# Kernel tuning notes

Measured on AMD Instinct MI355X. Metric: run time of the kernel, lower is better.

## Reference

```python
import jax, jax.numpy as jnp
import numpy as np

NUM_HEADS = 16
HEAD_DIM = 64
CONTEXT = 128


def setup_inputs() -> dict:
    key = jax.random.key(0)
    k1, k2, k3, k4, k5 = jax.random.split(key, 5)
    B, S, H = 4, 4096, 1024
    inputs = jax.random.normal(k1, (B, S, H), dtype=jnp.float32)
    attention_mask = jnp.ones((B, S), dtype=jnp.int32)
    s = 1.0 / np.sqrt(H)
    Wq = jax.random.normal(k2, (H, H), dtype=jnp.float32) * s
    Wk = jax.random.normal(k3, (H, H), dtype=jnp.float32) * s
    Wv = jax.random.normal(k4, (H, H), dtype=jnp.float32) * s
    Wo = jax.random.normal(k5, (H, H), dtype=jnp.float32) * s
    return {"inputs": inputs, "attention_mask": attention_mask,
            "Wq": Wq, "Wk": Wk, "Wv": Wv, "Wo": Wo}


def reference(inputs, attention_mask, Wq, Wk, Wv, Wo):
    B, S, H = inputs.shape
    nH, dh = NUM_HEADS, HEAD_DIM
    C = min(CONTEXT, S)
    ctx_start = max(0, S - C)
    scale = 1.0 / np.sqrt(dh)

    # Q from all positions; K/V only from the recent context window
    q = (inputs @ Wq.T).reshape(B, S, nH, dh).transpose(0, 2, 1, 3)      # [B,nH,S,dh]
    ctx_in = inputs[:, ctx_start:, :]                                    # [B,C,H]
    k = (ctx_in @ Wk.T).reshape(B, C, nH, dh).transpose(0, 2, 1, 3)      # [B,nH,C,dh]
    v = (ctx_in @ Wv.T).reshape(B, C, nH, dh).transpose(0, 2, 1, 3)      # [B,nH,C,dh]

    scores = jnp.einsum('bhsd,bhcd->bhsc', q, k) * scale                 # [B,nH,S,C]

    # causal mask: context position <= query position; queries strictly
    # before the context window may attend to the first context token
    qpos = jnp.arange(S)
    cpos = jnp.arange(ctx_start, ctx_start + C)
    causal = cpos[None, :] <= qpos[:, None]                              # [S,C]
    before = qpos < ctx_start
    causal = causal.at[:, 0].set(causal[:, 0] | before)
    mask = causal[None, None, :, :]                                      # [1,1,S,C]

    # padding mask on context tokens
    ctx_pad = (attention_mask[:, ctx_start:ctx_start + C] != 0)          # [B,C]
    mask = mask & ctx_pad[:, None, None, :]

    scores = jnp.where(mask, scores, -jnp.inf)
    weights = jax.nn.softmax(scores, axis=-1)

    out = jnp.einsum('bhsc,bhcd->bhsd', weights, v)                      # [B,nH,S,dh]
    out = out.transpose(0, 2, 1, 3).reshape(B, S, H)
    return out @ Wo.T
```

## Files before the change

### kernel.cpp

```cpp
#include <hip/hip_runtime.h>
#include <math.h>

#define B_ 4
#define S_ 4096
#define H_ 1024
#define NH 16
#define DH 64
#define CTX 128
#define CSTART (S_ - CTX)
#define KDIM 1024
#define KH 512

typedef __attribute__((ext_vector_type(8))) short short8;
typedef __attribute__((ext_vector_type(4))) float floatx4;
typedef unsigned short ushort_t;

__device__ inline unsigned short f2bf(float x) {
    union { float f; unsigned u; } v; v.f = x;
    unsigned r = v.u + 0x7fffu + ((v.u >> 16) & 1u);
    return (unsigned short)(r >> 16);
}

__device__ inline uint4 pack8(float4 a, float4 b) {
    union { unsigned short us[8]; uint4 u4; } p;
    p.us[0]=f2bf(a.x); p.us[1]=f2bf(a.y); p.us[2]=f2bf(a.z); p.us[3]=f2bf(a.w);
    p.us[4]=f2bf(b.x); p.us[5]=f2bf(b.y); p.us[6]=f2bf(b.z); p.us[7]=f2bf(b.w);
    return p.u4;
}

__device__ inline float4 add4(float4 a, float4 b) {
    float4 r; r.x=a.x+b.x; r.y=a.y+b.y; r.z=a.z+b.z; r.w=a.w+b.w; return r;
}

#define GLOAD_LDS16(g, l) \
    __builtin_amdgcn_global_load_lds((__attribute__((address_space(1))) const void*)(g), \
                                     (__attribute__((address_space(3))) void*)(l), 16, 0, 0)

__global__ __launch_bounds__(256) void prep(const float* __restrict__ in,
                                            const float* __restrict__ Wq, const float* __restrict__ Wk,
                                            const float* __restrict__ Wv, const float* __restrict__ Wo,
                                            ushort_t* __restrict__ Wbf, ushort_t* __restrict__ Xs) {
    int bx = blockIdx.x;
    if (bx < 2048) {
        size_t idx = (size_t)bx * 256 + threadIdx.x;
        size_t e = idx * 8;
        int wsel = (int)(e >> 20);
        size_t off = e & 1048575;
        const float* src = wsel == 0 ? Wq : wsel == 1 ? Wk : wsel == 2 ? Wv : Wo;
        const float4* s4 = (const float4*)(src + off);
        *(uint4*)(Wbf + e) = pack8(s4[0], s4[1]);
    } else {
        int idx = (bx - 2048) * 256 + threadIdx.x;
        int e = idx * 8;
        int m = e >> 10;
        int col = e & 1023;
        int b = m >> 7, i = m & 127;
        const float4* s4 = (const float4*)(in + (size_t)(b * S_ + CSTART + i) * H_ + col);
        *(uint4*)(Xs + e) = pack8(s4[0], s4[1]);
    }
}

__global__ __launch_bounds__(256) void gemm_part(const ushort_t* __restrict__ A,
                                                 const ushort_t* __restrict__ W,
                                                 float* __restrict__ P, int N) {
    __shared__ ushort_t As[64][64];
    __shared__ ushort_t Bs[64][64];
    int tid = threadIdx.x;
    int lane = tid & 63, w = tid >> 6;
    int m0 = blockIdx.y * 64, n0 = blockIdx.x * 64;
    int ks = blockIdx.z;
    int f0 = tid, f1 = tid + 256;
    int r0 = f0 >> 3, g0 = (f0 & 7) ^ (r0 & 7);
    int r1 = f1 >> 3, g1 = (f1 & 7) ^ (r1 & 7);
    const ushort_t* ga0 = A + (size_t)(m0 + r0) * KDIM + ks * KH + g0 * 8;
    const ushort_t* ga1 = A + (size_t)(m0 + r1) * KDIM + ks * KH + g1 * 8;
    const ushort_t* gb0 = W + (size_t)(n0 + r0) * KDIM + ks * KH + g0 * 8;
    const ushort_t* gb1 = W + (size_t)(n0 + r1) * KDIM + ks * KH + g1 * 8;
    char* la0 = (char*)As + f0 * 16;
    char* la1 = (char*)As + f1 * 16;
    char* lb0 = (char*)Bs + f0 * 16;
    char* lb1 = (char*)Bs + f1 * 16;
    int fm = lane & 15, q = lane >> 4;
    int wr = w >> 1, wc = w & 1;
    int ma0 = wr * 32, na0 = wc * 32;
    floatx4 acc[2][2] = {};
    for (int k0 = 0; k0 < KH; k0 += 64) {
        GLOAD_LDS16(ga0 + k0, la0);
        GLOAD_LDS16(ga1 + k0, la1);
        GLOAD_LDS16(gb0 + k0, lb0);
        GLOAD_LDS16(gb1 + k0, lb1);
        __syncthreads();
        #pragma unroll
        for (int kb = 0; kb < 2; kb++) {
            short8 af[2], bfr[2];
            #pragma unroll
            for (int t = 0; t < 2; t++) {
                int m = ma0 + t * 16 + fm;
                int pa = (kb * 4 + q) ^ (m & 7);
                af[t] = *(const short8*)&As[m][pa * 8];
                int n = na0 + t * 16 + fm;
                int pb = (kb * 4 + q) ^ (n & 7);
                bfr[t] = *(const short8*)&Bs[n][pb * 8];
            }
            #pragma unroll
            for (int i = 0; i < 2; i++)
                #pragma unroll
                for (int j = 0; j < 2; j++)
                    acc[i][j] = __builtin_amdgcn_mfma_f32_16x16x32_bf16(af[i], bfr[j], acc[i][j], 0, 0, 0);
        }
        __syncthreads();
    }
    float* outp = P + (size_t)ks * 512 * N;
    #pragma unroll
    for (int i = 0; i < 2; i++)
        #pragma unroll
        for (int j = 0; j < 2; j++) {
            int row = m0 + ma0 + i * 16 + q * 4;
            int col = n0 + na0 + j * 16 + fm;
            #pragma unroll
            for (int t = 0; t < 4; t++)
                outp[(size_t)(row + t) * N + col] = acc[i][j][t];
        }
}

__global__ __launch_bounds__(256) void attn(const float* __restrict__ Pq,
                                            const int* __restrict__ amask,
                                            ushort_t* __restrict__ AO) {
    __shared__ __align__(16) char smem[46080];
    ushort_t* Qs   = (ushort_t*)(smem);
    ushort_t* Ksh  = (ushort_t*)(smem + 9216);
    ushort_t* Pb   = (ushort_t*)(smem);
    float*    linv = (float*)(smem + 27648);
    int*      amk  = (int*)(smem + 27904);
    ushort_t* Vt   = (ushort_t*)(smem + 28416);

    int gid = blockIdx.x;
    int b = gid >> 5, h = (gid >> 1) & 15, half = gid & 1;
    int tid = threadIdx.x;
    int cmax = half ? CTX : 64;
    {
        int r = tid >> 2, ch = tid & 3;
        size_t qb = (size_t)(b * CTX + half * 64 + r) * 3072 + h * 64 + ch * 16;
        const float4* q0 = (const float4*)(Pq + qb);
        const float4* q1 = (const float4*)(Pq + (size_t)512 * 3072 + qb);
        float4 a0 = add4(q0[0], q1[0]), a1 = add4(q0[1], q1[1]);
        float4 a2 = add4(q0[2], q1[2]), a3 = add4(q0[3], q1[3]);
        *(uint4*)(Qs + r * 72 + ch * 16)     = pack8(a0, a1);
        *(uint4*)(Qs + r * 72 + ch * 16 + 8) = pack8(a2, a3);
        for (int idx = tid; idx < cmax * 4; idx += 256) {
            int kr = idx >> 2, kch = idx & 3;
            size_t base = (size_t)(b * CTX + kr) * 3072 + h * 64 + kch * 16;
            const float4* p0 = (const float4*)(Pq + base);
            const float4* p1 = (const float4*)(Pq + (size_t)512 * 3072 + base);
            float4 k0 = add4(p0[256], p1[256]), k1 = add4(p0[257], p1[257]);
            float4 k2 = add4(p0[258], p1[258]), k3 = add4(p0[259], p1[259]);
            *(uint4*)(Ksh + kr * 72 + kch * 16)     = pack8(k0, k1);
            *(uint4*)(Ksh + kr * 72 + kch * 16 + 8) = pack8(k2, k3);
            float vv[16];
            #pragma unroll
            for (int c4 = 0; c4 < 4; c4++) {
                float4 s = add4(p0[512 + c4], p1[512 + c4]);
                vv[c4*4+0]=s.x; vv[c4*4+1]=s.y; vv[c4*4+2]=s.z; vv[c4*4+3]=s.w;
            }
            #pragma unroll
            for (int i = 0; i < 16; i++)
                Vt[(kch * 16 + i) * 136 + kr] = f2bf(vv[i]);
        }
        if (tid < 128) amk[tid] = amask[b * S_ + CSTART + tid];
    }
    __syncthreads();

    int w = tid >> 6, lane = tid & 63;
    int qt = half * 4 + w;
    int lr0 = w * 16;
    int fm = lane & 15, quad = lane >> 4;

    short8 af[2];
    #pragma unroll
    for (int kb = 0; kb < 2; kb++)
        af[kb] = *(const short8*)(Qs + (lr0 + fm) * 72 + kb * 32 + quad * 8);
    floatx4 acc[8] = {};
    for (int ct = 0; ct <= qt; ct++) {
        #pragma unroll
        for (int kb = 0; kb < 2; kb++) {
            short8 bfr = *(const short8*)(Ksh + (ct * 16 + fm) * 72 + kb * 32 + quad * 8);
            acc[ct] = __builtin_amdgcn_mfma_f32_16x16x32_bf16(af[kb], bfr, acc[ct], 0, 0, 0);
        }
    }
    int myamk[8];
    #pragma unroll
    for (int ct = 0; ct < 8; ct++) myamk[ct] = amk[ct * 16 + fm];
    float ls[4];
    #pragma unroll
    for (int t = 0; t < 4; t++) {
        int row = qt * 16 + quad * 4 + t;
        float m = -INFINITY;
        #pragma unroll
        for (int ct = 0; ct < 8; ct++) {
            int col = ct * 16 + fm;
            float s = acc[ct][t] * 0.125f;
            bool valid = (ct <= qt) && (col <= row) && (myamk[ct] != 0);
            if (valid) m = fmaxf(m, s);
        }
        #pragma unroll
        for (int off = 8; off >= 1; off >>= 1) m = fmaxf(m, __shfl_xor(m, off, 64));
        float l = 0.f;
        #pragma unroll
        for (int ct = 0; ct < 8; ct++) {
            int col = ct * 16 + fm;
            float s = acc[ct][t] * 0.125f;
            bool valid = (ct <= qt) && (col <= row) && (myamk[ct] != 0);
            float p = valid ? __expf(s - m) : 0.f;
            acc[ct][t] = p;
            l += p;
        }
        #pragma unroll
        for (int off = 8; off >= 1; off >>= 1) l += __shfl_xor(l, off, 64);
        ls[t] = l;
    }
    __syncthreads();
    #pragma unroll
    for (int t = 0; t < 4; t++) {
        int lrow = lr0 + quad * 4 + t;
        #pragma unroll
        for (int ct = 0; ct < 8; ct++)
            Pb[lrow * 136 + ct * 16 + fm] = f2bf(acc[ct][t]);
        if (fm == 0) linv[lrow] = 1.f / ls[t];
    }
    int kmax = (qt >> 1) + 1;
    floatx4 oacc[4] = {};
    for (int kb = 0; kb < kmax; kb++) {
        short8 paf = *(const short8*)(Pb + (lr0 + fm) * 136 + kb * 32 + quad * 8);
        #pragma unroll
        for (int dt = 0; dt < 4; dt++) {
            short8 vbf = *(const short8*)(Vt + (dt * 16 + fm) * 136 + kb * 32 + quad * 8);
            oacc[dt] = __builtin_amdgcn_mfma_f32_16x16x32_bf16(paf, vbf, oacc[dt], 0, 0, 0);
        }
    }
    #pragma unroll
    for (int t = 0; t < 4; t++) {
        int lrow = lr0 + quad * 4 + t;
        int grow = qt * 16 + quad * 4 + t;
        float inv = linv[lrow];
        #pragma unroll
        for (int dt = 0; dt < 4; dt++)
            AO[(size_t)(b * CTX + grow) * H_ + h * 64 + dt * 16 + fm] = f2bf(oacc[dt][t] * inv);
    }
}

__global__ __launch_bounds__(256) void assemble(const float* __restrict__ Po,
                                                float* __restrict__ out) {
    size_t idx = (size_t)blockIdx.x * 256 + threadIdx.x;
    int row = (int)(idx >> 8);
    int c4  = (int)(idx & 255);
    int b = row >> 12;
    int p = row & 4095;
    int lr = (p < CSTART) ? 0 : (p - CSTART);
    size_t o = (size_t)(b * CTX + lr) * H_ + c4 * 4;
    float4 v0 = *(const float4*)(Po + o);
    float4 v1 = *(const float4*)(Po + (size_t)512 * H_ + o);
    ((float4*)out)[idx] = add4(v0, v1);
}

extern "C" void kernel_launch(void* const* d_in, const int* in_sizes, int n_in,
                              void* d_out, int out_size, void* d_ws, size_t ws_size,
                              hipStream_t stream) {
    const float* inputs = (const float*)d_in[0];
    const int*   amask  = (const int*)d_in[1];
    const float* Wq     = (const float*)d_in[2];
    const float* Wk     = (const float*)d_in[3];
    const float* Wv     = (const float*)d_in[4];
    const float* Wo     = (const float*)d_in[5];
    float* out = (float*)d_out;

    char* ws = (char*)d_ws;
    ushort_t* Xs   = (ushort_t*)(ws);
    ushort_t* Wbf  = (ushort_t*)(ws + (1u << 20));
    float*    Pq   = (float*)(ws + (9u << 20));
    ushort_t* AObf = (ushort_t*)(ws + (23u << 20));
    float*    Po   = (float*)(ws + (24u << 20));

    prep<<<2304, 256, 0, stream>>>(inputs, Wq, Wk, Wv, Wo, Wbf, Xs);

    dim3 gq(3072 / 64, 512 / 64, 2);
    gemm_part<<<gq, 256, 0, stream>>>(Xs, Wbf, Pq, 3072);

    attn<<<128, 256, 0, stream>>>(Pq, amask, AObf);

    dim3 go(1024 / 64, 512 / 64, 2);
    gemm_part<<<go, 256, 0, stream>>>(AObf, Wbf + (size_t)3072 * 1024, Po, 1024);

    assemble<<<16384, 256, 0, stream>>>(Po, out);
}
```

Before: 151.8 us.

## Fuse all stages into one cooperative persistent kernel with grid syncs

Replaces the five separate launches (prep, QKV GEMM, attention, output GEMM, assemble) with a single cooperative kernel of 512 blocks that separates the phases with grid.sync(). The output projection now runs the full K=1024 in one tile and writes straight into the context rows of the output, so the split-K partial buffer and its reduction disappear. The final phase broadcasts the position-0 context row to every earlier position. This removes launch gaps and one intermediate buffer, but adds grid-wide barrier costs, leaves most blocks idle during the attention and output phases, and needs all 512 blocks to be co-resident.

```diff
diff --git a/kernel.cpp b/kernel.cpp
--- a/kernel.cpp
+++ b/kernel.cpp
@@ -1,5 +1,8 @@
 #include <hip/hip_runtime.h>
+#include <hip/hip_cooperative_groups.h>
 #include <math.h>
+
+namespace cg = cooperative_groups;
 
 #define B_ 4
 #define S_ 4096
@@ -36,55 +39,32 @@
     __builtin_amdgcn_global_load_lds((__attribute__((address_space(1))) const void*)(g), \
                                      (__attribute__((address_space(3))) void*)(l), 16, 0, 0)
 
-__global__ __launch_bounds__(256) void prep(const float* __restrict__ in,
-                                            const float* __restrict__ Wq, const float* __restrict__ Wk,
-                                            const float* __restrict__ Wv, const float* __restrict__ Wo,
-                                            ushort_t* __restrict__ Wbf, ushort_t* __restrict__ Xs) {
-    int bx = blockIdx.x;
-    if (bx < 2048) {
-        size_t idx = (size_t)bx * 256 + threadIdx.x;
-        size_t e = idx * 8;
-        int wsel = (int)(e >> 20);
-        size_t off = e & 1048575;
-        const float* src = wsel == 0 ? Wq : wsel == 1 ? Wk : wsel == 2 ? Wv : Wo;
-        const float4* s4 = (const float4*)(src + off);
-        *(uint4*)(Wbf + e) = pack8(s4[0], s4[1]);
-    } else {
-        int idx = (bx - 2048) * 256 + threadIdx.x;
-        int e = idx * 8;
-        int m = e >> 10;
-        int col = e & 1023;
-        int b = m >> 7, i = m & 127;
-        const float4* s4 = (const float4*)(in + (size_t)(b * S_ + CSTART + i) * H_ + col);
-        *(uint4*)(Xs + e) = pack8(s4[0], s4[1]);
-    }
-}
-
-__global__ __launch_bounds__(256) void gemm_part(const ushort_t* __restrict__ A,
-                                                 const ushort_t* __restrict__ W,
-                                                 float* __restrict__ P, int N) {
-    __shared__ ushort_t As[64][64];
-    __shared__ ushort_t Bs[64][64];
-    int tid = threadIdx.x;
+template<bool DIRECT, int KLEN>
+__device__ __forceinline__ void gemm_tile(const ushort_t* __restrict__ A,
+                                          const ushort_t* __restrict__ W,
+                                          float* __restrict__ P, int N,
+                                          int m0, int n0, int koff,
+                                          char* smem, int tid) {
+    ushort_t* As = (ushort_t*)smem;
+    ushort_t* Bs = As + 4096;
     int lane = tid & 63, w = tid >> 6;
-    int m0 = blockIdx.y * 64, n0 = blockIdx.x * 64;
-    int ks = blockIdx.z;
     int f0 = tid, f1 = tid + 256;
     int r0 = f0 >> 3, g0 = (f0 & 7) ^ (r0 & 7);
     int r1 = f1 >> 3, g1 = (f1 & 7) ^ (r1 & 7);
-    const ushort_t* ga0 = A + (size_t)(m0 + r0) * KDIM + ks * KH + g0 * 8;
-    const ushort_t* ga1 = A + (size_t)(m0 + r1) * KDIM + ks * KH + g1 * 8;
-    const ushort_t* gb0 = W + (size_t)(n0 + r0) * KDIM + ks * KH + g0 * 8;
-    const ushort_t* gb1 = W + (size_t)(n0 + r1) * KDIM + ks * KH + g1 * 8;
-    char* la0 = (char*)As + f0 * 16;
-    char* la1 = (char*)As + f1 * 16;
-    char* lb0 = (char*)Bs + f0 * 16;
-    char* lb1 = (char*)Bs + f1 * 16;
+    const ushort_t* ga0 = A + (size_t)(m0 + r0) * KDIM + koff + g0 * 8;
+    const ushort_t* ga1 = A + (size_t)(m0 + r1) * KDIM + koff + g1 * 8;
+    const ushort_t* gb0 = W + (size_t)(n0 + r0) * KDIM + koff + g0 * 8;
+    const ushort_t* gb1 = W + (size_t)(n0 + r1) * KDIM + koff + g1 * 8;
+    char* la0 = smem + f0 * 16;
+    char* la1 = smem + f1 * 16;
+    char* lb0 = smem + 8192 + f0 * 16;
+    char* lb1 = smem + 8192 + f1 * 16;
     int fm = lane & 15, q = lane >> 4;
     int wr = w >> 1, wc = w & 1;
     int ma0 = wr * 32, na0 = wc * 32;
     floatx4 acc[2][2] = {};
-    for (int k0 = 0; k0 < KH; k0 += 64) {
+    #pragma unroll
+    for (int k0 = 0; k0 < KLEN; k0 += 64) {
         GLOAD_LDS16(ga0 + k0, la0);
         GLOAD_LDS16(ga1 + k0, la1);
         GLOAD_LDS16(gb0 + k0, lb0);
@@ -97,10 +77,10 @@
             for (int t = 0; t < 2; t++) {
                 int m = ma0 + t * 16 + fm;
                 int pa = (kb * 4 + q) ^ (m & 7);
-                af[t] = *(const short8*)&As[m][pa * 8];
+                af[t] = *(const short8*)(As + m * 64 + pa * 8);
                 int n = na0 + t * 16 + fm;
                 int pb = (kb * 4 + q) ^ (n & 7);
-                bfr[t] = *(const short8*)&Bs[n][pb * 8];
+                bfr[t] = *(const short8*)(Bs + n * 64 + pb * 8);
             }
             #pragma unroll
             for (int i = 0; i < 2; i++)
@@ -110,7 +90,6 @@
         }
         __syncthreads();
     }
-    float* outp = P + (size_t)ks * 512 * N;
     #pragma unroll
     for (int i = 0; i < 2; i++)
         #pragma unroll
@@ -118,15 +97,22 @@
             int row = m0 + ma0 + i * 16 + q * 4;
             int col = n0 + na0 + j * 16 + fm;
             #pragma unroll
-            for (int t = 0; t < 4; t++)
-                outp[(size_t)(row + t) * N + col] = acc[i][j][t];
-        }
-}
-
-__global__ __launch_bounds__(256) void attn(const float* __restrict__ Pq,
-                                            const int* __restrict__ amask,
-                                            ushort_t* __restrict__ AO) {
-    __shared__ __align__(16) char smem[46080];
+            for (int t = 0; t < 4; t++) {
+                int rr = row + t;
+                if (DIRECT) {
+                    size_t gr = (size_t)((rr >> 7) * S_ + CSTART + (rr & 127));
+                    P[gr * 1024 + col] = acc[i][j][t];
+                } else {
+                    P[(size_t)rr * N + col] = acc[i][j][t];
+                }
+            }
+        }
+}
+
+__device__ __forceinline__ void attn_body(const float* __restrict__ Pq,
+                                          const int* __restrict__ amask,
+                                          ushort_t* __restrict__ AO,
+                                          char* smem, int gid) {
     ushort_t* Qs   = (ushort_t*)(smem);
     ushort_t* Ksh  = (ushort_t*)(smem + 9216);
     ushort_t* Pb   = (ushort_t*)(smem);
@@ -134,7 +120,6 @@
     int*      amk  = (int*)(smem + 27904);
     ushort_t* Vt   = (ushort_t*)(smem + 28416);
 
-    int gid = blockIdx.x;
     int b = gid >> 5, h = (gid >> 1) & 15, half = gid & 1;
     int tid = threadIdx.x;
     int cmax = half ? CTX : 64;
@@ -248,18 +233,67 @@
     }
 }
 
-__global__ __launch_bounds__(256) void assemble(const float* __restrict__ Po,
+__global__ __launch_bounds__(256, 2) void fused(const float* __restrict__ in,
+                                                const int* __restrict__ amask,
+                                                const float* __restrict__ Wq, const float* __restrict__ Wk,
+                                                const float* __restrict__ Wv, const float* __restrict__ Wo,
+                                                ushort_t* __restrict__ Wbf, ushort_t* __restrict__ Xs,
+                                                float* __restrict__ Pq, ushort_t* __restrict__ AObf,
                                                 float* __restrict__ out) {
-    size_t idx = (size_t)blockIdx.x * 256 + threadIdx.x;
-    int row = (int)(idx >> 8);
-    int c4  = (int)(idx & 255);
-    int b = row >> 12;
-    int p = row & 4095;
-    int lr = (p < CSTART) ? 0 : (p - CSTART);
-    size_t o = (size_t)(b * CTX + lr) * H_ + c4 * 4;
-    float4 v0 = *(const float4*)(Po + o);
-    float4 v1 = *(const float4*)(Po + (size_t)512 * H_ + o);
-    ((float4*)out)[idx] = add4(v0, v1);
+    __shared__ __align__(16) char smem[46080];
+    cg::grid_group grid = cg::this_grid();
+    int bid = blockIdx.x, tid = threadIdx.x;
+
+    for (unsigned u = (unsigned)bid * 256 + tid; u < 589824u; u += 131072u) {
+        size_t e = (size_t)u * 8;
+        if (u < 524288u) {
+            int wsel = (int)(e >> 20);
+            size_t off = e & 1048575;
+            const float* src = wsel == 0 ? Wq : wsel == 1 ? Wk : wsel == 2 ? Wv : Wo;
+            const float4* s4 = (const float4*)(src + off);
+            *(uint4*)(Wbf + e) = pack8(s4[0], s4[1]);
+        } else {
+            size_t e2 = e - 4194304;
+            int m = (int)(e2 >> 10), col = (int)(e2 & 1023);
+            int b2 = m >> 7, i = m & 127;
+            const float4* s4 = (const float4*)(in + (size_t)(b2 * S_ + CSTART + i) * H_ + col);
+            *(uint4*)(Xs + e2) = pack8(s4[0], s4[1]);
+        }
+    }
+    grid.sync();
+
+    {
+        int job = bid;
+        int x = job % 48, y = (job / 48) & 7, z = job / 384;
+        gemm_tile<false, KH>(Xs, Wbf, Pq + (size_t)z * 512 * 3072, 3072,
+                             y * 64, x * 64, z * KH, smem, tid);
+        if (bid < 256) {
+            int j2 = bid + 512;
+            int x2 = j2 % 48, y2 = (j2 / 48) & 7, z2 = j2 / 384;
+            gemm_tile<false, KH>(Xs, Wbf, Pq + (size_t)z2 * 512 * 3072, 3072,
+                                 y2 * 64, x2 * 64, z2 * KH, smem, tid);
+        }
+    }
+    grid.sync();
+
+    if (bid < 128) attn_body(Pq, amask, AObf, smem, bid);
+    grid.sync();
+
+    if (bid < 128) {
+        int x = bid % 16, y = bid / 16;
+        gemm_tile<true, 1024>(AObf, Wbf + (size_t)3072 * 1024, out, 1024,
+                              y * 64, x * 64, 0, smem, tid);
+    }
+    grid.sync();
+
+    for (unsigned idx = (unsigned)bid * 256 + tid; idx < 4063232u; idx += 131072u) {
+        unsigned b2 = idx / 1015808u;
+        unsigned rem = idx - b2 * 1015808u;
+        unsigned p = rem >> 8;
+        unsigned c4 = rem & 255u;
+        float4 v = *(const float4*)(out + (size_t)(b2 * S_ + CSTART) * H_ + c4 * 4);
+        ((float4*)out)[(size_t)(b2 * S_ + p) * 256 + c4] = v;
+    }
 }
 
 extern "C" void kernel_launch(void* const* d_in, const int* in_sizes, int n_in,
@@ -278,17 +312,19 @@
     ushort_t* Wbf  = (ushort_t*)(ws + (1u << 20));
     float*    Pq   = (float*)(ws + (9u << 20));
     ushort_t* AObf = (ushort_t*)(ws + (23u << 20));
-    float*    Po   = (float*)(ws + (24u << 20));
-
-    prep<<<2304, 256, 0, stream>>>(inputs, Wq, Wk, Wv, Wo, Wbf, Xs);
-
-    dim3 gq(3072 / 64, 512 / 64, 2);
-    gemm_part<<<gq, 256, 0, stream>>>(Xs, Wbf, Pq, 3072);
-
-    attn<<<128, 256, 0, stream>>>(Pq, amask, AObf);
-
-    dim3 go(1024 / 64, 512 / 64, 2);
-    gemm_part<<<go, 256, 0, stream>>>(AObf, Wbf + (size_t)3072 * 1024, Po, 1024);
-
-    assemble<<<16384, 256, 0, stream>>>(Po, out);
-}
+
+    void* args[11];
+    args[0]  = (void*)&inputs;
+    args[1]  = (void*)&amask;
+    args[2]  = (void*)&Wq;
+    args[3]  = (void*)&Wk;
+    args[4]  = (void*)&Wv;
+    args[5]  = (void*)&Wo;
+    args[6]  = (void*)&Wbf;
+    args[7]  = (void*)&Xs;
+    args[8]  = (void*)&Pq;
+    args[9]  = (void*)&AObf;
+    args[10] = (void*)&out;
+
+    hipLaunchCooperativeKernel((const void*)fused, dim3(512), dim3(256), args, 0, stream);
+}
```

After: 406.6 us. 2.68x slower.

## Fuse bf16 conversion into GEMMs and fuse output projection with broadcast write

Applied to the files above, without the earlier changes.

Drops the separate prep kernel and converts fp32 inputs and weights to bf16 while staging tiles into shared memory, using register prefetch of the next k-tile. The output projection now runs over the full K in one pass and writes the 512 context rows straight into the output. Extra blocks compute the single shared row for pre-context positions as a dot-product GEMV and broadcast it across those rows, which removes the split-K partial buffer and the assemble kernel. In exchange the GEMM loops do conversion work inline, and the broadcast rows use a scalar per-element bf16 path.

```diff
diff --git a/kernel.cpp b/kernel.cpp
--- a/kernel.cpp
+++ b/kernel.cpp
@@ -9,7 +9,6 @@
 #define CTX 128
 #define CSTART (S_ - CTX)
 #define KDIM 1024
-#define KH 512
 
 typedef __attribute__((ext_vector_type(8))) short short8;
 typedef __attribute__((ext_vector_type(4))) float floatx4;
@@ -19,6 +18,10 @@
     union { float f; unsigned u; } v; v.f = x;
     unsigned r = v.u + 0x7fffu + ((v.u >> 16) & 1u);
     return (unsigned short)(r >> 16);
+}
+
+__device__ inline float bf2f(ushort_t u) {
+    union { unsigned u; float f; } v; v.u = ((unsigned)u) << 16; return v.f;
 }
 
 __device__ inline uint4 pack8(float4 a, float4 b) {
@@ -36,60 +39,56 @@
     __builtin_amdgcn_global_load_lds((__attribute__((address_space(1))) const void*)(g), \
                                      (__attribute__((address_space(3))) void*)(l), 16, 0, 0)
 
-__global__ __launch_bounds__(256) void prep(const float* __restrict__ in,
-                                            const float* __restrict__ Wq, const float* __restrict__ Wk,
-                                            const float* __restrict__ Wv, const float* __restrict__ Wo,
-                                            ushort_t* __restrict__ Wbf, ushort_t* __restrict__ Xs) {
-    int bx = blockIdx.x;
-    if (bx < 2048) {
-        size_t idx = (size_t)bx * 256 + threadIdx.x;
-        size_t e = idx * 8;
-        int wsel = (int)(e >> 20);
-        size_t off = e & 1048575;
-        const float* src = wsel == 0 ? Wq : wsel == 1 ? Wk : wsel == 2 ? Wv : Wo;
-        const float4* s4 = (const float4*)(src + off);
-        *(uint4*)(Wbf + e) = pack8(s4[0], s4[1]);
-    } else {
-        int idx = (bx - 2048) * 256 + threadIdx.x;
-        int e = idx * 8;
-        int m = e >> 10;
-        int col = e & 1023;
-        int b = m >> 7, i = m & 127;
-        const float4* s4 = (const float4*)(in + (size_t)(b * S_ + CSTART + i) * H_ + col);
-        *(uint4*)(Xs + e) = pack8(s4[0], s4[1]);
-    }
-}
-
-__global__ __launch_bounds__(256) void gemm_part(const ushort_t* __restrict__ A,
-                                                 const ushort_t* __restrict__ W,
-                                                 float* __restrict__ P, int N) {
+__global__ __launch_bounds__(256) void qkv_gemm(const float* __restrict__ in,
+                                                const float* __restrict__ Wq,
+                                                const float* __restrict__ Wk,
+                                                const float* __restrict__ Wv,
+                                                float* __restrict__ Pq) {
     __shared__ ushort_t As[64][64];
     __shared__ ushort_t Bs[64][64];
+    int bid = blockIdx.x;
+    int z = bid / 384;
+    int rem = bid - z * 384;
+    int x = rem % 48, y = rem / 48;
+    int m0 = y * 64, n0 = x * 64, koff = z * 512;
+    const float* Wsrc = (n0 < 1024) ? Wq : (n0 < 2048) ? Wk : Wv;
+    int nrow0 = n0 & 1023;
+
     int tid = threadIdx.x;
     int lane = tid & 63, w = tid >> 6;
-    int m0 = blockIdx.y * 64, n0 = blockIdx.x * 64;
-    int ks = blockIdx.z;
-    int f0 = tid, f1 = tid + 256;
-    int r0 = f0 >> 3, g0 = (f0 & 7) ^ (r0 & 7);
-    int r1 = f1 >> 3, g1 = (f1 & 7) ^ (r1 & 7);
-    const ushort_t* ga0 = A + (size_t)(m0 + r0) * KDIM + ks * KH + g0 * 8;
-    const ushort_t* ga1 = A + (size_t)(m0 + r1) * KDIM + ks * KH + g1 * 8;
-    const ushort_t* gb0 = W + (size_t)(n0 + r0) * KDIM + ks * KH + g0 * 8;
-    const ushort_t* gb1 = W + (size_t)(n0 + r1) * KDIM + ks * KH + g1 * 8;
-    char* la0 = (char*)As + f0 * 16;
-    char* la1 = (char*)As + f1 * 16;
-    char* lb0 = (char*)Bs + f0 * 16;
-    char* lb1 = (char*)Bs + f1 * 16;
+    int r0 = tid >> 3, g0 = (tid & 7) ^ (r0 & 7);
+    int r1 = r0 + 32,  g1 = (tid & 7) ^ (r1 & 7);
+
+    int am0 = m0 + r0, am1 = m0 + r1;
+    const float* gaA0 = in + (size_t)((am0 >> 7) * S_ + CSTART + (am0 & 127)) * H_ + koff + g0 * 8;
+    const float* gaA1 = in + (size_t)((am1 >> 7) * S_ + CSTART + (am1 & 127)) * H_ + koff + g1 * 8;
+    const float* gaB0 = Wsrc + (size_t)(nrow0 + r0) * 1024 + koff + g0 * 8;
+    const float* gaB1 = Wsrc + (size_t)(nrow0 + r1) * 1024 + koff + g1 * 8;
+    uint4* lsA0 = (uint4*)((char*)As + tid * 16);
+    uint4* lsA1 = (uint4*)((char*)As + tid * 16 + 4096);
+    uint4* lsB0 = (uint4*)((char*)Bs + tid * 16);
+    uint4* lsB1 = (uint4*)((char*)Bs + tid * 16 + 4096);
+
     int fm = lane & 15, q = lane >> 4;
     int wr = w >> 1, wc = w & 1;
     int ma0 = wr * 32, na0 = wc * 32;
     floatx4 acc[2][2] = {};
-    for (int k0 = 0; k0 < KH; k0 += 64) {
-        GLOAD_LDS16(ga0 + k0, la0);
-        GLOAD_LDS16(ga1 + k0, la1);
-        GLOAD_LDS16(gb0 + k0, lb0);
-        GLOAD_LDS16(gb1 + k0, lb1);
+
+    float4 ra0, ra1, ra2, ra3, rb0, rb1, rb2, rb3;
+#define LOAD_REGS_K1(k) do { \
+        ra0 = *(const float4*)(gaA0 + (k));     ra1 = *(const float4*)(gaA0 + (k) + 4); \
+        ra2 = *(const float4*)(gaA1 + (k));     ra3 = *(const float4*)(gaA1 + (k) + 4); \
+        rb0 = *(const float4*)(gaB0 + (k));     rb1 = *(const float4*)(gaB0 + (k) + 4); \
+        rb2 = *(const float4*)(gaB1 + (k));     rb3 = *(const float4*)(gaB1 + (k) + 4); } while (0)
+
+    LOAD_REGS_K1(0);
+    for (int k0 = 0; k0 < 512; k0 += 64) {
+        uint4 pa0 = pack8(ra0, ra1), pa1 = pack8(ra2, ra3);
+        uint4 pb0 = pack8(rb0, rb1), pb1 = pack8(rb2, rb3);
+        if (k0) __syncthreads();
+        *lsA0 = pa0; *lsA1 = pa1; *lsB0 = pb0; *lsB1 = pb1;
         __syncthreads();
+        if (k0 + 64 < 512) LOAD_REGS_K1(k0 + 64);
         #pragma unroll
         for (int kb = 0; kb < 2; kb++) {
             short8 af[2], bfr[2];
@@ -97,10 +96,10 @@
             for (int t = 0; t < 2; t++) {
                 int m = ma0 + t * 16 + fm;
                 int pa = (kb * 4 + q) ^ (m & 7);
-                af[t] = *(const short8*)&As[m][pa * 8];
+                af[t] = *(const short8*)(&As[m][pa * 8]);
                 int n = na0 + t * 16 + fm;
                 int pb = (kb * 4 + q) ^ (n & 7);
-                bfr[t] = *(const short8*)&Bs[n][pb * 8];
+                bfr[t] = *(const short8*)(&Bs[n][pb * 8]);
             }
             #pragma unroll
             for (int i = 0; i < 2; i++)
@@ -108,9 +107,8 @@
                 for (int j = 0; j < 2; j++)
                     acc[i][j] = __builtin_amdgcn_mfma_f32_16x16x32_bf16(af[i], bfr[j], acc[i][j], 0, 0, 0);
         }
-        __syncthreads();
-    }
-    float* outp = P + (size_t)ks * 512 * N;
+    }
+    float* outp = Pq + (size_t)z * 512 * 3072;
     #pragma unroll
     for (int i = 0; i < 2; i++)
         #pragma unroll
@@ -119,7 +117,7 @@
             int col = n0 + na0 + j * 16 + fm;
             #pragma unroll
             for (int t = 0; t < 4; t++)
-                outp[(size_t)(row + t) * N + col] = acc[i][j][t];
+                outp[(size_t)(row + t) * 3072 + col] = acc[i][j][t];
         }
 }
 
@@ -248,18 +246,120 @@
     }
 }
 
-__global__ __launch_bounds__(256) void assemble(const float* __restrict__ Po,
-                                                float* __restrict__ out) {
-    size_t idx = (size_t)blockIdx.x * 256 + threadIdx.x;
-    int row = (int)(idx >> 8);
-    int c4  = (int)(idx & 255);
-    int b = row >> 12;
-    int p = row & 4095;
-    int lr = (p < CSTART) ? 0 : (p - CSTART);
-    size_t o = (size_t)(b * CTX + lr) * H_ + c4 * 4;
-    float4 v0 = *(const float4*)(Po + o);
-    float4 v1 = *(const float4*)(Po + (size_t)512 * H_ + o);
-    ((float4*)out)[idx] = add4(v0, v1);
+__global__ __launch_bounds__(256) void ogemm_bcast(const ushort_t* __restrict__ AObf,
+                                                   const float* __restrict__ Wo,
+                                                   float* __restrict__ out) {
+    __shared__ __align__(16) char smem[16384];
+    int bid = blockIdx.x;
+    int tid = threadIdx.x;
+
+    if (bid < 128) {
+        ushort_t (*As)[64] = (ushort_t(*)[64])smem;
+        ushort_t (*Bs)[64] = (ushort_t(*)[64])(smem + 8192);
+        int x = bid % 16, y = bid / 16;
+        int m0 = y * 64, n0 = x * 64;
+        int lane = tid & 63, w = tid >> 6;
+        int r0 = tid >> 3, g0 = (tid & 7) ^ (r0 & 7);
+        int r1 = r0 + 32,  g1 = (tid & 7) ^ (r1 & 7);
+        const ushort_t* ga0 = AObf + (size_t)(m0 + r0) * KDIM + g0 * 8;
+        const ushort_t* ga1 = AObf + (size_t)(m0 + r1) * KDIM + g1 * 8;
+        const float*    gb0 = Wo + (size_t)(n0 + r0) * 1024 + g0 * 8;
+        const float*    gb1 = Wo + (size_t)(n0 + r1) * 1024 + g1 * 8;
+        char* laA0 = smem + tid * 16;
+        char* laA1 = smem + tid * 16 + 4096;
+        uint4* lsB0 = (uint4*)(smem + 8192 + tid * 16);
+        uint4* lsB1 = (uint4*)(smem + 8192 + tid * 16 + 4096);
+
+        int fm = lane & 15, q = lane >> 4;
+        int wr = w >> 1, wc = w & 1;
+        int ma0 = wr * 32, na0 = wc * 32;
+        floatx4 acc[2][2] = {};
+
+        float4 rb0, rb1, rb2, rb3;
+#define LOAD_REGS_K3(k) do { \
+            rb0 = *(const float4*)(gb0 + (k)); rb1 = *(const float4*)(gb0 + (k) + 4); \
+            rb2 = *(const float4*)(gb1 + (k)); rb3 = *(const float4*)(gb1 + (k) + 4); } while (0)
+
+        LOAD_REGS_K3(0);
+        for (int k0 = 0; k0 < 1024; k0 += 64) {
+            uint4 pb0 = pack8(rb0, rb1), pb1 = pack8(rb2, rb3);
+            if (k0) __syncthreads();
+            GLOAD_LDS16(ga0 + k0, laA0);
+            GLOAD_LDS16(ga1 + k0, laA1);
+            *lsB0 = pb0; *lsB1 = pb1;
+            __syncthreads();
+            if (k0 + 64 < 1024) LOAD_REGS_K3(k0 + 64);
+            #pragma unroll
+            for (int kb = 0; kb < 2; kb++) {
+                short8 af[2], bfr[2];
+                #pragma unroll
+                for (int t = 0; t < 2; t++) {
+                    int m = ma0 + t * 16 + fm;
+                    int pa = (kb * 4 + q) ^ (m & 7);
+                    af[t] = *(const short8*)(&As[m][pa * 8]);
+                    int n = na0 + t * 16 + fm;
+                    int pb = (kb * 4 + q) ^ (n & 7);
+                    bfr[t] = *(const short8*)(&Bs[n][pb * 8]);
+                }
+                #pragma unroll
+                for (int i = 0; i < 2; i++)
+                    #pragma unroll
+                    for (int j = 0; j < 2; j++)
+                        acc[i][j] = __builtin_amdgcn_mfma_f32_16x16x32_bf16(af[i], bfr[j], acc[i][j], 0, 0, 0);
+            }
+        }
+        #pragma unroll
+        for (int i = 0; i < 2; i++)
+            #pragma unroll
+            for (int j = 0; j < 2; j++) {
+                int row = m0 + ma0 + i * 16 + q * 4;
+                int col = n0 + na0 + j * 16 + fm;
+                #pragma unroll
+                for (int t = 0; t < 4; t++) {
+                    int rr = row + t;
+                    size_t gr = (size_t)((rr >> 7) * S_ + CSTART + (rr & 127));
+                    out[gr * 1024 + col] = acc[i][j][t];
+                }
+            }
+    } else {
+        float* vals = (float*)smem;
+        int idx = bid - 128;
+        int c  = idx & 15;
+        int b2 = (idx >> 4) & 3;
+        int rc = idx >> 6;
+        int n0 = c * 64;
+        int w = tid >> 6, lane = tid & 63;
+        int rsub = lane >> 4, kl = lane & 15;
+        const ushort_t* ao = AObf + (size_t)(b2 * 128) * 1024;
+        #pragma unroll
+        for (int p = 0; p < 4; p++) {
+            int rl = p * 16 + w * 4 + rsub;
+            const float* wrow = Wo + (size_t)(n0 + rl) * 1024;
+            float4 av = {0.f, 0.f, 0.f, 0.f};
+            #pragma unroll
+            for (int it = 0; it < 16; it++) {
+                int k = kl * 4 + it * 64;
+                float4 wv = *(const float4*)(wrow + k);
+                av.x += wv.x * bf2f(ao[k]);
+                av.y += wv.y * bf2f(ao[k + 1]);
+                av.z += wv.z * bf2f(ao[k + 2]);
+                av.w += wv.w * bf2f(ao[k + 3]);
+            }
+            float s = av.x + av.y + av.z + av.w;
+            #pragma unroll
+            for (int off = 1; off < 16; off <<= 1) s += __shfl_xor(s, off, 64);
+            if (kl == 0) vals[rl] = s;
+        }
+        __syncthreads();
+        int c4 = tid & 15, ro = tid >> 4;
+        float4 v4 = *(const float4*)(vals + c4 * 4);
+        size_t gbase = (size_t)b2 * S_ * 1024 + n0 + c4 * 4;
+        #pragma unroll
+        for (int i = 0; i < 31; i++) {
+            int p = rc * 496 + ro + i * 16;
+            *(float4*)(out + gbase + (size_t)p * 1024) = v4;
+        }
+    }
 }
 
 extern "C" void kernel_launch(void* const* d_in, const int* in_sizes, int n_in,
@@ -274,21 +374,10 @@
     float* out = (float*)d_out;
 
     char* ws = (char*)d_ws;
-    ushort_t* Xs   = (ushort_t*)(ws);
-    ushort_t* Wbf  = (ushort_t*)(ws + (1u << 20));
-    float*    Pq   = (float*)(ws + (9u << 20));
-    ushort_t* AObf = (ushort_t*)(ws + (23u << 20));
-    float*    Po   = (float*)(ws + (24u << 20));
-
-    prep<<<2304, 256, 0, stream>>>(inputs, Wq, Wk, Wv, Wo, Wbf, Xs);
-
-    dim3 gq(3072 / 64, 512 / 64, 2);
-    gemm_part<<<gq, 256, 0, stream>>>(Xs, Wbf, Pq, 3072);
-
+    float*    Pq   = (float*)(ws);
+    ushort_t* AObf = (ushort_t*)(ws + (13u << 20));
+
+    qkv_gemm<<<768, 256, 0, stream>>>(inputs, Wq, Wk, Wv, Pq);
     attn<<<128, 256, 0, stream>>>(Pq, amask, AObf);
-
-    dim3 go(1024 / 64, 512 / 64, 2);
-    gemm_part<<<go, 256, 0, stream>>>(AObf, Wbf + (size_t)3072 * 1024, Po, 1024);
-
-    assemble<<<16384, 256, 0, stream>>>(Po, out);
-}
+    ogemm_bcast<<<640, 256, 0, stream>>>(AObf, Wo, out);
+}
```

Result: slower. 155.8 us (+2.6%).
